# Kernel tuning notes

Measured on AMD Instinct MI355X. Metric: run time of the kernel, lower is better.

The kernel has to match this reference:

```python
import jax, jax.numpy as jnp
import numpy as np


def setup_inputs() -> dict:
    key = jax.random.key(0)
    ks = jax.random.split(key, 5)
    B, C, H, W = 16, 256, 96, 96
    NODES, HID = 7, 256
    return {
        "input": jax.random.normal(ks[0], (1, B, NODES, HID), dtype=jnp.float32),
        "res_feature": jax.random.normal(ks[1], (B, C, H, W), dtype=jnp.float32),
        "node_fea_for_res": jax.random.normal(ks[2], (C, 1), dtype=jnp.float32) * (1.0 / np.sqrt(C)),
        "node_fea_for_hidden": jax.random.normal(ks[3], (HID, 1), dtype=jnp.float32) * (1.0 / np.sqrt(HID)),
        "weight": jax.random.normal(ks[4], (HID, C), dtype=jnp.float32) * (1.0 / np.sqrt(HID)),
    }


def reference(input, res_feature, node_fea_for_res, node_fea_for_hidden, weight):
    # input: (1, B, N, HID); res_feature: (B, C, H, W)
    B, C, H, W = res_feature.shape
    x = input[0]                                   # (B, N, HID)
    res = res_feature.reshape(B, C, H * W)         # (B, C, P)
    # Per-pixel score (broadcast over nodes) and per-node score (broadcast over pixels).
    # Equivalent to the original expand+matmul without materializing (B,P,N,C)/(B,P,N,HID).
    s_res = jnp.einsum('bcp,c->bp', res, node_fea_for_res[:, 0])    # (B, P)
    s_hid = jnp.einsum('bnh,h->bn', x, node_fea_for_hidden[:, 0])   # (B, N)
    scores = s_res[:, :, None] + s_hid[:, None, :]                  # (B, P, N)
    attn = jax.nn.softmax(scores, axis=-1)                          # softmax over nodes
    node_vals = jnp.einsum('bnh,hc->bnc', x, weight)                # (B, N, C)
    out = jnp.einsum('bpn,bnc->bcp', attn, node_vals)               # (B, C, P)
    return jax.nn.relu(out.reshape(B, C, H, W))
```

## Files before the change

### kernel.cpp

```cpp
#include <hip/hip_runtime.h>
#include <math.h>


#define B 16
#define NODES 7
#define HID 256
#define C 256
#define P 9216
#define P4 2304

__global__ __launch_bounds__(256) void compute_M(
    const float* __restrict__ x,
    const float* __restrict__ nfh,
    const float* __restrict__ W,
    float* __restrict__ M) {
  const int b = blockIdx.x;
  const int t = threadIdx.x;
  const int lane = t & 63;
  const int wave = t >> 6;

  __shared__ float xs[NODES * HID];
  __shared__ float red[NODES][4];
  __shared__ float a[NODES];
  __shared__ float y[HID];

#pragma unroll
  for (int n = 0; n < NODES; ++n)
    xs[n * HID + t] = x[((size_t)b * NODES + n) * HID + t];
  const float f = nfh[t];
  __syncthreads();

#pragma unroll
  for (int n = 0; n < NODES; ++n) {
    float v = xs[n * HID + t] * f;
#pragma unroll
    for (int off = 32; off > 0; off >>= 1) v += __shfl_down(v, off, 64);
    if (lane == 0) red[n][wave] = v;
  }
  __syncthreads();

  if (t == 0) {
    float s[NODES];
    float m = -3.0e38f;
#pragma unroll
    for (int n = 0; n < NODES; ++n) {
      s[n] = red[n][0] + red[n][1] + red[n][2] + red[n][3];
      m = fmaxf(m, s[n]);
    }
    float denom = 0.0f;
#pragma unroll
    for (int n = 0; n < NODES; ++n) {
      s[n] = expf(s[n] - m);
      denom += s[n];
    }
    const float inv = 1.0f / denom;
#pragma unroll
    for (int n = 0; n < NODES; ++n) a[n] = s[n] * inv;
  }
  __syncthreads();

  float yv = 0.0f;
#pragma unroll
  for (int n = 0; n < NODES; ++n) yv = fmaf(a[n], xs[n * HID + t], yv);
  y[t] = yv;
  __syncthreads();

  float acc = 0.0f;
#pragma unroll 8
  for (int h = 0; h < HID; ++h) acc = fmaf(y[h], W[h * C + t], acc);
  M[b * C + t] = fmaxf(acc, 0.0f);
}

__global__ __launch_bounds__(256) void broadcast_fill(
    const float* __restrict__ M,
    float* __restrict__ out) {
  const int bc = blockIdx.x;
  const float v = M[bc];
  const float4 v4 = make_float4(v, v, v, v);
  float4* dst = reinterpret_cast<float4*>(out) + (size_t)bc * P4;
  const int t = threadIdx.x;
#pragma unroll
  for (int i = 0; i < 9; ++i) dst[i * 256 + t] = v4;
}

extern "C" void kernel_launch(void* const* d_in, const int* in_sizes, int n_in,
                              void* d_out, int out_size, void* d_ws, size_t ws_size,
                              hipStream_t stream) {
  const float* x   = (const float*)d_in[0];
  const float* nfh = (const float*)d_in[3];
  const float* W   = (const float*)d_in[4];
  float* out = (float*)d_out;
  float* M = (float*)d_ws;

  compute_M<<<B, 256, 0, stream>>>(x, nfh, W, M);
  broadcast_fill<<<B * C, 256, 0, stream>>>(M, out);
}
```

Measured before the change: 247.1 us.

## Fuse attention-vector computation into the broadcast fill kernel

```diff
diff --git a/kernel.cpp b/kernel.cpp
--- a/kernel.cpp
+++ b/kernel.cpp
@@ -9,12 +9,14 @@
 #define P 9216
 #define P4 2304
 
-__global__ __launch_bounds__(256) void compute_M(
+__global__ __launch_bounds__(256) void fused_attn_fill(
     const float* __restrict__ x,
     const float* __restrict__ nfh,
     const float* __restrict__ W,
-    float* __restrict__ M) {
-  const int b = blockIdx.x;
+    float* __restrict__ out) {
+  const int bc = blockIdx.x;
+  const int b = bc >> 8;
+  const int c = bc & (C - 1);
   const int t = threadIdx.x;
   const int lane = t & 63;
   const int wave = t >> 6;
@@ -22,12 +24,14 @@
   __shared__ float xs[NODES * HID];
   __shared__ float red[NODES][4];
   __shared__ float a[NODES];
-  __shared__ float y[HID];
+  __shared__ float red2[4];
+  __shared__ float Msh;
 
 #pragma unroll
   for (int n = 0; n < NODES; ++n)
     xs[n * HID + t] = x[((size_t)b * NODES + n) * HID + t];
   const float f = nfh[t];
+  const float wcol = W[t * C + c];
   __syncthreads();
 
 #pragma unroll
@@ -62,23 +66,18 @@
   float yv = 0.0f;
 #pragma unroll
   for (int n = 0; n < NODES; ++n) yv = fmaf(a[n], xs[n * HID + t], yv);
-  y[t] = yv;
+  float p = yv * wcol;
+
+#pragma unroll
+  for (int off = 32; off > 0; off >>= 1) p += __shfl_down(p, off, 64);
+  if (lane == 0) red2[wave] = p;
+  __syncthreads();
+  if (t == 0) Msh = fmaxf(red2[0] + red2[1] + red2[2] + red2[3], 0.0f);
   __syncthreads();
 
-  float acc = 0.0f;
-#pragma unroll 8
-  for (int h = 0; h < HID; ++h) acc = fmaf(y[h], W[h * C + t], acc);
-  M[b * C + t] = fmaxf(acc, 0.0f);
-}
-
-__global__ __launch_bounds__(256) void broadcast_fill(
-    const float* __restrict__ M,
-    float* __restrict__ out) {
-  const int bc = blockIdx.x;
-  const float v = M[bc];
+  const float v = Msh;
   const float4 v4 = make_float4(v, v, v, v);
   float4* dst = reinterpret_cast<float4*>(out) + (size_t)bc * P4;
-  const int t = threadIdx.x;
 #pragma unroll
   for (int i = 0; i < 9; ++i) dst[i * 256 + t] = v4;
 }
@@ -90,8 +89,6 @@
   const float* nfh = (const float*)d_in[3];
   const float* W   = (const float*)d_in[4];
   float* out = (float*)d_out;
-  float* M = (float*)d_ws;
 
-  compute_M<<<B, 256, 0, stream>>>(x, nfh, W, M);
-  broadcast_fill<<<B * C, 256, 0, stream>>>(M, out);
+  fused_attn_fill<<<B * C, 256, 0, stream>>>(x, nfh, W, out);
 }
```

After: 235.1 us. -4.9%, faster.
